# Kernel optimization log

Hardware: AMD Instinct MI355X
Metric: run time of the kernel (lower is better)

Reference implementation:

```python
import jax, jax.numpy as jnp
import numpy as np

B, T, C, H = 2, 512, 64, 64  # batch, seq (<= block_size), n_embd, head_size


def setup_inputs() -> dict:
    key = jax.random.key(0)
    ks = jax.random.split(key, 9)
    p = lambda k, sh: jax.random.normal(k, sh, jnp.float32) * 0.02
    return {
        "x": jax.random.normal(ks[0], (B, T, C), jnp.float32),
        "pos_emb": jax.random.normal(ks[1], (T, C), jnp.float32),
        "pos_dist_emb": jax.random.normal(ks[2], (B, T, T, 2 * C), jnp.float32),
        # GeluFeedForward(4c -> c -> 1): Linear(4c, c) -> GELU -> Linear(c, 1)
        "W1": p(ks[3], (4 * C, C)),
        "b1": p(ks[4], (C,)),
        "W2": p(ks[5], (C, 1)),
        "b2": p(ks[6], (1,)),
        # value projection Linear(c, head_size)
        "Wv": p(ks[7], (C, H)),
        "bv": p(ks[8], (H,)),
    }


def reference(x, pos_emb, pos_dist_emb, W1, b1, W2, b2, Wv, bv):
    b, t, c = x.shape
    x1 = x + pos_emb  # (b,t,c)
    # cat([k, q, pos_dist], -1) @ W1 == k@W1[:c] + q@W1[c:2c] + pd@W1[2c:]
    # (avoids materializing the (b,t,t,4c) repeat+cat tensor; same math)
    W1k, W1q, W1p = W1[:c], W1[c:2 * c], W1[2 * c:]
    kp = x1 @ W1k                 # (b,t,c): key side, varies over pair axis 2
    qp = x1 @ W1q                 # (b,t,c): query side, varies over pair axis 1
    pp = pos_dist_emb @ W1p       # (b,t,t,c)
    h = jax.nn.gelu(qp[:, :, None, :] + kp[:, None, :, :] + pp + b1,
                    approximate=False)          # (b,t,t,c)
    wei = ((h @ W2)[..., 0] + b2[0]) * (c ** -0.5)  # (b,t,t)
    causal = jnp.tril(jnp.ones((t, t), bool))
    wei = jnp.where(causal, wei, -jnp.inf)
    wei = jax.nn.softmax(wei, axis=-1)          # (b,t,t); dropout p=0
    v = x @ Wv + bv                             # (b,t,H)
    return wei @ v                              # (b,t,H)
```

## Files before the change

kernel.cpp:

```cpp
#include <hip/hip_runtime.h>
#include <math.h>

#define BB 2
#define TT 512
#define CC 64
#define HH 64
#define KK 128
#define JT 64

typedef __attribute__((ext_vector_type(8))) short short8;
typedef __attribute__((ext_vector_type(4))) float float4v;

__device__ inline unsigned short f2bf(float f) {
    unsigned int u = __float_as_uint(f);
    u = (u + 0x7FFFu + ((u >> 16) & 1u)) >> 16;
    return (unsigned short)u;
}

__device__ inline short8 cvt8(float4 a, float4 b) {
    short8 r;
    r[0] = (short)f2bf(a.x); r[1] = (short)f2bf(a.y);
    r[2] = (short)f2bf(a.z); r[3] = (short)f2bf(a.w);
    r[4] = (short)f2bf(b.x); r[5] = (short)f2bf(b.y);
    r[6] = (short)f2bf(b.z); r[7] = (short)f2bf(b.w);
    return r;
}

__global__ __launch_bounds__(256) void pack_kernel(
    const float* __restrict__ W1, unsigned short* __restrict__ Wpt)
{
    int t = blockIdx.x * 256 + threadIdx.x;
    int c = t >> 7;
    int k = t & 127;
    Wpt[c * KK + k] = f2bf(W1[(2 * CC + k) * CC + c]);
}

__global__ __launch_bounds__(64) void prep_kernel(
    const float* __restrict__ x, const float* __restrict__ pos_emb,
    const float* __restrict__ W1, const float* __restrict__ b1,
    const float* __restrict__ Wv, const float* __restrict__ bv,
    float* __restrict__ kp, float* __restrict__ qpb, float* __restrict__ v)
{
    const int row = blockIdx.x;
    const int t = row & (TT - 1);
    const int c = threadIdx.x;
    __shared__ float xs[CC], x1s[CC];
    float xv = x[row * CC + c];
    xs[c] = xv;
    x1s[c] = xv + pos_emb[t * CC + c];
    __syncthreads();
    float ak = 0.f, aq = 0.f, av = 0.f;
#pragma unroll 8
    for (int k = 0; k < CC; ++k) {
        ak = fmaf(x1s[k], W1[k * CC + c], ak);
        aq = fmaf(x1s[k], W1[(CC + k) * CC + c], aq);
        av = fmaf(xs[k], Wv[k * HH + c], av);
    }
    kp[row * CC + c] = ak;
    qpb[row * CC + c] = aq + b1[c];
    v[row * HH + c] = av + bv[c];
}

__global__ __launch_bounds__(256) void wei_kernel(
    const float* __restrict__ pd, const unsigned short* __restrict__ Wpt,
    const float* __restrict__ W2, const float* __restrict__ b2,
    const float* __restrict__ kp, const float* __restrict__ qpb,
    float* __restrict__ wei)
{
    const int i = blockIdx.y;
    const int b = blockIdx.z;
    const int j0 = blockIdx.x * JT;
    if (j0 > i) return;

    const int tid = threadIdx.x;
    const int wave = tid >> 6;
    const int lane = tid & 63;
    const int m = lane & 15;
    const int kg = lane >> 4;

    const int jrow = j0 + wave * 16 + m;
    const float* __restrict__ arow =
        pd + (((size_t)b * TT + i) * TT + jrow) * KK + kg * 8;

    float4 av[8];
#pragma unroll
    for (int kt = 0; kt < 4; ++kt) {
        av[2 * kt]     = *(const float4*)(arow + kt * 32);
        av[2 * kt + 1] = *(const float4*)(arow + kt * 32 + 4);
    }

    float4v acc[4] = {{0.f,0.f,0.f,0.f},{0.f,0.f,0.f,0.f},
                      {0.f,0.f,0.f,0.f},{0.f,0.f,0.f,0.f}};
#pragma unroll
    for (int kt = 0; kt < 4; ++kt) {
        short8 a = cvt8(av[2 * kt], av[2 * kt + 1]);
#pragma unroll
        for (int nt = 0; nt < 4; ++nt) {
            short8 bf = *(const short8*)&Wpt[(nt * 16 + m) * KK + kt * 32 + kg * 8];
            acc[nt] = __builtin_amdgcn_mfma_f32_16x16x32_bf16(a, bf, acc[nt], 0, 0, 0);
        }
    }

    float w2v[4], qv[4];
#pragma unroll
    for (int nt = 0; nt < 4; ++nt) {
        int c = nt * 16 + m;
        w2v[nt] = W2[c];
        qv[nt] = qpb[((size_t)b * TT + i) * CC + c];
    }
    const float b2v = b2[0];

#pragma unroll
    for (int r = 0; r < 4; ++r) {
        const int j = j0 + wave * 16 + kg * 4 + r;
        float s = 0.f;
#pragma unroll
        for (int nt = 0; nt < 4; ++nt) {
            float tv = acc[nt][r] + qv[nt] + kp[((size_t)b * TT + j) * CC + nt * 16 + m];
            float g = 0.5f * tv * (1.f + erff(tv * 0.70710678118654752f));
            s = fmaf(g, w2v[nt], s);
        }
#pragma unroll
        for (int off = 1; off < 16; off <<= 1) s += __shfl_xor(s, off);
        if (m == r && j <= i)
            wei[((size_t)b * TT + i) * TT + j] = (s + b2v) * 0.125f;
    }
}

__device__ inline float wave_reduce_max(float m) {
#pragma unroll
    for (int off = 32; off > 0; off >>= 1) m = fmaxf(m, __shfl_down(m, off));
    return m;
}
__device__ inline float wave_reduce_sum(float s) {
#pragma unroll
    for (int off = 32; off > 0; off >>= 1) s += __shfl_down(s, off);
    return s;
}

__global__ __launch_bounds__(256) void out_kernel(
    const float* __restrict__ wei, const float* __restrict__ v,
    float* __restrict__ out)
{
    const int i = blockIdx.x;
    const int b = blockIdx.y;
    const int tid = threadIdx.x;
    const int wv = tid >> 6;
    const int lane = tid & 63;
    const int n = i + 1;

    __shared__ float p[TT];
    __shared__ float red[4];
    __shared__ float part[4][HH];

    float m = -1e30f;
    for (int jj = tid; jj < n; jj += 256) {
        float w = wei[((size_t)b * TT + i) * TT + jj];
        p[jj] = w;
        m = fmaxf(m, w);
    }
    m = wave_reduce_max(m);
    if (lane == 0) red[wv] = m;
    __syncthreads();
    const float M = fmaxf(fmaxf(red[0], red[1]), fmaxf(red[2], red[3]));
    __syncthreads();

    float s = 0.f;
    for (int jj = tid; jj < n; jj += 256) {
        float e = __expf(p[jj] - M);
        p[jj] = e;
        s += e;
    }
    s = wave_reduce_sum(s);
    if (lane == 0) red[wv] = s;
    __syncthreads();
    const float S = red[0] + red[1] + red[2] + red[3];
    const float inv = 1.f / S;

    float a0 = 0.f, a1 = 0.f, a2 = 0.f, a3 = 0.f;
    int jj = wv;
    for (; jj + 12 < n; jj += 16) {
        a0 = fmaf(p[jj],      v[((size_t)b * TT + jj) * HH + lane], a0);
        a1 = fmaf(p[jj + 4],  v[((size_t)b * TT + jj + 4) * HH + lane], a1);
        a2 = fmaf(p[jj + 8],  v[((size_t)b * TT + jj + 8) * HH + lane], a2);
        a3 = fmaf(p[jj + 12], v[((size_t)b * TT + jj + 12) * HH + lane], a3);
    }
    for (; jj < n; jj += 4)
        a0 = fmaf(p[jj], v[((size_t)b * TT + jj) * HH + lane], a0);
    part[wv][lane] = a0 + a1 + a2 + a3;
    __syncthreads();
    if (tid < HH) {
        float r = (part[0][tid] + part[1][tid] + part[2][tid] + part[3][tid]) * inv;
        out[((size_t)b * TT + i) * HH + tid] = r;
    }
}

extern "C" void kernel_launch(void* const* d_in, const int* in_sizes, int n_in,
                              void* d_out, int out_size, void* d_ws, size_t ws_size,
                              hipStream_t stream)
{
    const float* x       = (const float*)d_in[0];
    const float* pos_emb = (const float*)d_in[1];
    const float* pd      = (const float*)d_in[2];
    const float* W1      = (const float*)d_in[3];
    const float* b1      = (const float*)d_in[4];
    const float* W2      = (const float*)d_in[5];
    const float* b2      = (const float*)d_in[6];
    const float* Wv      = (const float*)d_in[7];
    const float* bv      = (const float*)d_in[8];
    float* out = (float*)d_out;

    float* ws = (float*)d_ws;
    unsigned short* Wpt = (unsigned short*)ws;
    float* kp  = ws + 4096;
    float* qpb = ws + 4096 + 65536;
    float* v   = ws + 4096 + 131072;
    float* wei = ws + 4096 + 196608;

    pack_kernel<<<dim3(32), dim3(256), 0, stream>>>(W1, Wpt);
    prep_kernel<<<dim3(BB * TT), dim3(64), 0, stream>>>(x, pos_emb, W1, b1, Wv, bv, kp, qpb, v);
    wei_kernel<<<dim3(TT / JT, TT, BB), dim3(256), 0, stream>>>(pd, Wpt, W2, b2, kp, qpb, wei);
    out_kernel<<<dim3(TT, BB), dim3(256), 0, stream>>>(wei, v, out);
}
```

Measured before the change: 423.6 us.

## Fuse score and softmax-output kernels, fold key projection into MFMA K dimension

Merges the per-pair score kernel and the softmax/value kernel into one kernel per query row. Scores now stay in shared memory instead of going through a global wei buffer. The key-side projection is folded into the MFMA GEMM by appending bf16 x1 to the K dimension (K=192), with the weights staged once per block in padded LDS. It also software-pipelines the pos_dist loads across j tiles, replaces erff with a polynomial erf approximation, and pairs rows i and 511-i in launch order to balance causal work. The costs are lower precision from bf16 x1 and the approximate erf, plus a serial per-row loop that gives fewer blocks and less parallelism than before.

```diff
diff --git a/kernel.cpp b/kernel.cpp
--- a/kernel.cpp
+++ b/kernel.cpp
@@ -5,7 +5,9 @@
 #define TT 512
 #define CC 64
 #define HH 64
-#define KK 128
+#define KP 128
+#define KA 192
+#define PADB 198
 #define JT 64
 
 typedef __attribute__((ext_vector_type(8))) short short8;
@@ -26,20 +28,37 @@
     return r;
 }
 
+__device__ inline float gelu_erf(float x) {
+    float z = fabsf(x) * 0.70710678118654752f;
+    float t = __builtin_amdgcn_rcpf(fmaf(0.3275911f, z, 1.f));
+    float poly = fmaf(fmaf(fmaf(fmaf(1.061405429f, t, -1.453152027f),
+                                t, 1.421413741f),
+                           t, -0.284496736f),
+                      t, 0.254829592f) * t;
+    float erfc_ = poly * __expf(-z * z);
+    float onePlus = (x >= 0.f) ? (2.f - erfc_) : erfc_;
+    return 0.5f * x * onePlus;
+}
+
 __global__ __launch_bounds__(256) void pack_kernel(
-    const float* __restrict__ W1, unsigned short* __restrict__ Wpt)
+    const float* __restrict__ W1, unsigned short* __restrict__ Bext)
 {
     int t = blockIdx.x * 256 + threadIdx.x;
-    int c = t >> 7;
-    int k = t & 127;
-    Wpt[c * KK + k] = f2bf(W1[(2 * CC + k) * CC + c]);
+    if (t >= CC * PADB) return;
+    int c = t / PADB;
+    int k = t - c * PADB;
+    float val = 0.f;
+    if (k < 128)      val = W1[(2 * CC + k) * CC + c];
+    else if (k < 192) val = W1[(k - 128) * CC + c];
+    Bext[c * PADB + k] = f2bf(val);
 }
 
 __global__ __launch_bounds__(64) void prep_kernel(
     const float* __restrict__ x, const float* __restrict__ pos_emb,
     const float* __restrict__ W1, const float* __restrict__ b1,
     const float* __restrict__ Wv, const float* __restrict__ bv,
-    float* __restrict__ kp, float* __restrict__ qpb, float* __restrict__ v)
+    unsigned short* __restrict__ x1bf, float* __restrict__ qpb,
+    float* __restrict__ v)
 {
     const int row = blockIdx.x;
     const int t = row & (TT - 1);
@@ -47,60 +66,43 @@
     __shared__ float xs[CC], x1s[CC];
     float xv = x[row * CC + c];
     xs[c] = xv;
-    x1s[c] = xv + pos_emb[t * CC + c];
-    __syncthreads();
-    float ak = 0.f, aq = 0.f, av = 0.f;
+    float x1v = xv + pos_emb[t * CC + c];
+    x1s[c] = x1v;
+    __syncthreads();
+    float aq = 0.f, av = 0.f;
 #pragma unroll 8
     for (int k = 0; k < CC; ++k) {
-        ak = fmaf(x1s[k], W1[k * CC + c], ak);
         aq = fmaf(x1s[k], W1[(CC + k) * CC + c], aq);
         av = fmaf(xs[k], Wv[k * HH + c], av);
     }
-    kp[row * CC + c] = ak;
+    x1bf[row * CC + c] = f2bf(x1v);
     qpb[row * CC + c] = aq + b1[c];
     v[row * HH + c] = av + bv[c];
 }
 
-__global__ __launch_bounds__(256) void wei_kernel(
-    const float* __restrict__ pd, const unsigned short* __restrict__ Wpt,
+__global__ __launch_bounds__(256, 4) void attn_kernel(
+    const float* __restrict__ pd, const unsigned short* __restrict__ Bext,
+    const unsigned short* __restrict__ x1bf, const float* __restrict__ qpb,
     const float* __restrict__ W2, const float* __restrict__ b2,
-    const float* __restrict__ kp, const float* __restrict__ qpb,
-    float* __restrict__ wei)
-{
-    const int i = blockIdx.y;
-    const int b = blockIdx.z;
-    const int j0 = blockIdx.x * JT;
-    if (j0 > i) return;
-
+    const float* __restrict__ v, float* __restrict__ out)
+{
+    const int bx = blockIdx.x;
+    const int i = (bx < 256) ? bx : 767 - bx;
+    const int b = blockIdx.y;
     const int tid = threadIdx.x;
-    const int wave = tid >> 6;
-    const int lane = tid & 63;
-    const int m = lane & 15;
-    const int kg = lane >> 4;
-
-    const int jrow = j0 + wave * 16 + m;
-    const float* __restrict__ arow =
-        pd + (((size_t)b * TT + i) * TT + jrow) * KK + kg * 8;
-
-    float4 av[8];
-#pragma unroll
-    for (int kt = 0; kt < 4; ++kt) {
-        av[2 * kt]     = *(const float4*)(arow + kt * 32);
-        av[2 * kt + 1] = *(const float4*)(arow + kt * 32 + 4);
-    }
-
-    float4v acc[4] = {{0.f,0.f,0.f,0.f},{0.f,0.f,0.f,0.f},
-                      {0.f,0.f,0.f,0.f},{0.f,0.f,0.f,0.f}};
-#pragma unroll
-    for (int kt = 0; kt < 4; ++kt) {
-        short8 a = cvt8(av[2 * kt], av[2 * kt + 1]);
-#pragma unroll
-        for (int nt = 0; nt < 4; ++nt) {
-            short8 bf = *(const short8*)&Wpt[(nt * 16 + m) * KK + kt * 32 + kg * 8];
-            acc[nt] = __builtin_amdgcn_mfma_f32_16x16x32_bf16(a, bf, acc[nt], 0, 0, 0);
-        }
-    }
-
+    const int wave = tid >> 6, lane = tid & 63;
+    const int m = lane & 15, kg = lane >> 4;
+
+    __shared__ unsigned short Blds[CC * PADB];
+    __shared__ float p[TT];
+    __shared__ float red[4];
+    __shared__ float part[4][HH];
+
+    {
+        const uint4* __restrict__ src = (const uint4*)Bext;
+        uint4* dst = (uint4*)Blds;
+        for (int f = tid; f < (CC * PADB) / 8; f += 256) dst[f] = src[f];
+    }
     float w2v[4], qv[4];
 #pragma unroll
     for (int nt = 0; nt < 4; ++nt) {
@@ -109,76 +111,89 @@
         qv[nt] = qpb[((size_t)b * TT + i) * CC + c];
     }
     const float b2v = b2[0];
-
-#pragma unroll
-    for (int r = 0; r < 4; ++r) {
-        const int j = j0 + wave * 16 + kg * 4 + r;
-        float s = 0.f;
-#pragma unroll
-        for (int nt = 0; nt < 4; ++nt) {
-            float tv = acc[nt][r] + qv[nt] + kp[((size_t)b * TT + j) * CC + nt * 16 + m];
-            float g = 0.5f * tv * (1.f + erff(tv * 0.70710678118654752f));
-            s = fmaf(g, w2v[nt], s);
+    __syncthreads();
+
+    const int ntiles = (i + JT) / JT;
+    const int jrb = wave * 16 + m;
+    const float* __restrict__ pdb = pd + ((size_t)b * TT + i) * TT * KP;
+    const unsigned short* __restrict__ xb = x1bf + (size_t)b * TT * CC;
+
+    float4 av[8];
+    short8 ax[2];
+    auto load_tile = [&](int t) {
+        const float* __restrict__ ar = pdb + (size_t)(t * JT + jrb) * KP + kg * 8;
+#pragma unroll
+        for (int kt = 0; kt < 4; ++kt) {
+            av[2 * kt]     = *(const float4*)(ar + kt * 32);
+            av[2 * kt + 1] = *(const float4*)(ar + kt * 32 + 4);
         }
-#pragma unroll
-        for (int off = 1; off < 16; off <<= 1) s += __shfl_xor(s, off);
-        if (m == r && j <= i)
-            wei[((size_t)b * TT + i) * TT + j] = (s + b2v) * 0.125f;
-    }
-}
-
-__device__ inline float wave_reduce_max(float m) {
-#pragma unroll
-    for (int off = 32; off > 0; off >>= 1) m = fmaxf(m, __shfl_down(m, off));
-    return m;
-}
-__device__ inline float wave_reduce_sum(float s) {
-#pragma unroll
-    for (int off = 32; off > 0; off >>= 1) s += __shfl_down(s, off);
-    return s;
-}
-
-__global__ __launch_bounds__(256) void out_kernel(
-    const float* __restrict__ wei, const float* __restrict__ v,
-    float* __restrict__ out)
-{
-    const int i = blockIdx.x;
-    const int b = blockIdx.y;
-    const int tid = threadIdx.x;
-    const int wv = tid >> 6;
-    const int lane = tid & 63;
+        const unsigned short* __restrict__ xr = xb + (size_t)(t * JT + jrb) * CC + kg * 8;
+        ax[0] = *(const short8*)xr;
+        ax[1] = *(const short8*)(xr + 32);
+    };
+
+    load_tile(0);
+
+    for (int t = 0; t < ntiles; ++t) {
+        short8 af[6];
+#pragma unroll
+        for (int kt = 0; kt < 4; ++kt) af[kt] = cvt8(av[2 * kt], av[2 * kt + 1]);
+        af[4] = ax[0];
+        af[5] = ax[1];
+
+        if (t + 1 < ntiles) load_tile(t + 1);
+
+        float4v acc[4] = {{0.f,0.f,0.f,0.f},{0.f,0.f,0.f,0.f},
+                          {0.f,0.f,0.f,0.f},{0.f,0.f,0.f,0.f}};
+#pragma unroll
+        for (int kt = 0; kt < 6; ++kt) {
+#pragma unroll
+            for (int nt = 0; nt < 4; ++nt) {
+                short8 bf = *(const short8*)&Blds[(nt * 16 + m) * PADB + kt * 32 + kg * 8];
+                acc[nt] = __builtin_amdgcn_mfma_f32_16x16x32_bf16(af[kt], bf, acc[nt], 0, 0, 0);
+            }
+        }
+
+        const int j0 = t * JT + wave * 16 + kg * 4;
+#pragma unroll
+        for (int r = 0; r < 4; ++r) {
+            const int j = j0 + r;
+            float s = 0.f;
+#pragma unroll
+            for (int nt = 0; nt < 4; ++nt)
+                s = fmaf(gelu_erf(acc[nt][r] + qv[nt]), w2v[nt], s);
+#pragma unroll
+            for (int off = 1; off < 16; off <<= 1) s += __shfl_xor(s, off);
+            if (m == r)
+                p[j] = (j <= i) ? (s + b2v) * 0.125f : -1e30f;
+        }
+    }
+    __syncthreads();
+
     const int n = i + 1;
-
-    __shared__ float p[TT];
-    __shared__ float red[4];
-    __shared__ float part[4][HH];
-
-    float m = -1e30f;
-    for (int jj = tid; jj < n; jj += 256) {
-        float w = wei[((size_t)b * TT + i) * TT + jj];
-        p[jj] = w;
-        m = fmaxf(m, w);
-    }
-    m = wave_reduce_max(m);
-    if (lane == 0) red[wv] = m;
+    float mx = -1e30f;
+    for (int jj = tid; jj < n; jj += 256) mx = fmaxf(mx, p[jj]);
+#pragma unroll
+    for (int off = 32; off > 0; off >>= 1) mx = fmaxf(mx, __shfl_down(mx, off));
+    if (lane == 0) red[wave] = mx;
     __syncthreads();
     const float M = fmaxf(fmaxf(red[0], red[1]), fmaxf(red[2], red[3]));
     __syncthreads();
 
-    float s = 0.f;
+    float sm = 0.f;
     for (int jj = tid; jj < n; jj += 256) {
         float e = __expf(p[jj] - M);
         p[jj] = e;
-        s += e;
-    }
-    s = wave_reduce_sum(s);
-    if (lane == 0) red[wv] = s;
-    __syncthreads();
-    const float S = red[0] + red[1] + red[2] + red[3];
-    const float inv = 1.f / S;
+        sm += e;
+    }
+#pragma unroll
+    for (int off = 32; off > 0; off >>= 1) sm += __shfl_down(sm, off);
+    if (lane == 0) red[wave] = sm;
+    __syncthreads();
+    const float inv = 1.f / (red[0] + red[1] + red[2] + red[3]);
 
     float a0 = 0.f, a1 = 0.f, a2 = 0.f, a3 = 0.f;
-    int jj = wv;
+    int jj = wave;
     for (; jj + 12 < n; jj += 16) {
         a0 = fmaf(p[jj],      v[((size_t)b * TT + jj) * HH + lane], a0);
         a1 = fmaf(p[jj + 4],  v[((size_t)b * TT + jj + 4) * HH + lane], a1);
@@ -187,7 +202,7 @@
     }
     for (; jj < n; jj += 4)
         a0 = fmaf(p[jj], v[((size_t)b * TT + jj) * HH + lane], a0);
-    part[wv][lane] = a0 + a1 + a2 + a3;
+    part[wave][lane] = a0 + a1 + a2 + a3;
     __syncthreads();
     if (tid < HH) {
         float r = (part[0][tid] + part[1][tid] + part[2][tid] + part[3][tid]) * inv;
@@ -211,14 +226,12 @@
     float* out = (float*)d_out;
 
     float* ws = (float*)d_ws;
-    unsigned short* Wpt = (unsigned short*)ws;
-    float* kp  = ws + 4096;
-    float* qpb = ws + 4096 + 65536;
-    float* v   = ws + 4096 + 131072;
-    float* wei = ws + 4096 + 196608;
-
-    pack_kernel<<<dim3(32), dim3(256), 0, stream>>>(W1, Wpt);
-    prep_kernel<<<dim3(BB * TT), dim3(64), 0, stream>>>(x, pos_emb, W1, b1, Wv, bv, kp, qpb, v);
-    wei_kernel<<<dim3(TT / JT, TT, BB), dim3(256), 0, stream>>>(pd, Wpt, W2, b2, kp, qpb, wei);
-    out_kernel<<<dim3(TT, BB), dim3(256), 0, stream>>>(wei, v, out);
-}
+    unsigned short* Bext = (unsigned short*)ws;
+    unsigned short* x1bf = (unsigned short*)(ws + 6400);
+    float* qpb = ws + 6400 + 32768;
+    float* v   = ws + 6400 + 32768 + 65536;
+
+    pack_kernel<<<dim3((CC * PADB + 255) / 256), dim3(256), 0, stream>>>(W1, Bext);
+    prep_kernel<<<dim3(BB * TT), dim3(64), 0, stream>>>(x, pos_emb, W1, b1, Wv, bv, x1bf, qpb, v);
+    attn_kernel<<<dim3(TT, BB), dim3(256), 0, stream>>>(pd, Bext, x1bf, qpb, W2, b2, v, out);
+}
```

Result: no change. 417.8 us (-1.4%).
